# Kernel tuning notes

Hardware: AMD Instinct MI355X
Metric: run time of the kernel (lower is better)

## Reference

```python
import jax, jax.numpy as jnp
import numpy as np
from jax import lax

NUM_HEADS = 8
HEAD_DIM = 32
DIM = NUM_HEADS * HEAD_DIM  # 256
SR = 2
B, H, W = 4, 64, 64


def setup_inputs() -> dict:
    key = jax.random.key(0)
    ks = jax.random.split(key, 6)
    x = jax.random.normal(ks[0], (B, DIM, H, W), dtype=jnp.float32)
    # query: 1x1 conv without bias -> plain [out,in] matrix
    Wq = jax.random.normal(ks[1], (DIM, DIM), dtype=jnp.float32) * (1.0 / np.sqrt(DIM))
    # key/value: sr x sr conv, stride sr, no bias (OIHW)
    Wk = jax.random.normal(ks[2], (DIM, DIM, SR, SR), dtype=jnp.float32) * (1.0 / np.sqrt(DIM * SR * SR))
    Wv = jax.random.normal(ks[3], (DIM, DIM, SR, SR), dtype=jnp.float32) * (1.0 / np.sqrt(DIM * SR * SR))
    rel_h = jax.random.normal(ks[4], (1, NUM_HEADS, HEAD_DIM, 1, H // SR), dtype=jnp.float32)
    rel_w = jax.random.normal(ks[5], (1, NUM_HEADS, HEAD_DIM, W // SR, 1), dtype=jnp.float32)
    return {"x": x, "Wq": Wq, "Wk": Wk, "Wv": Wv, "rel_h": rel_h, "rel_w": rel_w}


def reference(x, Wq, Wk, Wv, rel_h, rel_w):
    b, c, h, w = x.shape
    nh, hd = NUM_HEADS, HEAD_DIM
    scale = hd ** (-0.5)
    dn = ('NCHW', 'OIHW', 'NCHW')

    # q: 1x1 conv == channel matmul; [B, C, H*W] -> [B, nh, hd, Nq]
    q = jnp.einsum('oc,bchw->bohw', Wq, x).reshape(b, nh, hd, h * w)
    # k, v: sr x sr conv, stride sr -> [B, nh, hd, Nkv]
    k = lax.conv_general_dilated(x, Wk, window_strides=(SR, SR), padding='VALID',
                                 dimension_numbers=dn).reshape(b, nh, hd, -1)
    v = lax.conv_general_dilated(x, Wv, window_strides=(SR, SR), padding='VALID',
                                 dimension_numbers=dn).reshape(b, nh, hd, -1)

    # attn scores: q^T k -> [B, nh, Nq, Nkv]
    attn = jnp.einsum('bhdn,bhdm->bhnm', q, k)
    # relative positional bias: (rel_h + rel_w) broadcast -> [nh, hd, Nkv]
    pos = (rel_h + rel_w).reshape(nh, hd, -1)
    attn = attn + jnp.einsum('bhdn,hdm->bhnm', q, pos)
    attn = jax.nn.softmax(attn * scale, axis=-1)

    # out = v @ attn^T -> [B, nh, hd, Nq] -> [B, C, H, W]
    out = jnp.einsum('bhdm,bhnm->bhdn', v, attn).reshape(b, c, h, w)
    return out
```

## Files before the change

kernel.cpp:

```cpp
#include <hip/hip_runtime.h>
#include <math.h>


typedef __bf16 bf16;
typedef __attribute__((ext_vector_type(4))) __bf16 bf16x4;
typedef __attribute__((ext_vector_type(8))) __bf16 bf16x8;
typedef __attribute__((ext_vector_type(4))) float f32x4;
typedef __attribute__((ext_vector_type(2))) __fp16 fp16x2_raw;
typedef __attribute__((ext_vector_type(4))) _Float16 f16x4;

#define MFMA16 __builtin_amdgcn_mfma_f32_16x16x32_bf16
#define MFMA16H __builtin_amdgcn_mfma_f32_16x16x16f16

#define QSCALE 0.25503486f
#define SOFTMAX_SHIFT 10.0f

__global__ void k_prep_w(const float* __restrict__ Wq, const float* __restrict__ Wk,
                         const float* __restrict__ Wv,
                         bf16* __restrict__ Wq_bf, bf16* __restrict__ Wkv_bf) {
    int tid = blockIdx.x * 256 + threadIdx.x;
    int c = tid >> 8, i = tid & 255;
    const float* Wsrc = (c < 256) ? Wk : Wv;
    int cs = c & 255;
    f32x4 w4 = ((const f32x4*)Wsrc)[cs * 256 + i];
#pragma unroll
    for (int tap = 0; tap < 4; tap++)
        Wkv_bf[c * 1024 + tap * 256 + i] = (bf16)w4[tap];
    if (tid < 16384) {
        f32x4 q4 = ((const f32x4*)Wq)[tid];
        bf16x4 o;
#pragma unroll
        for (int e = 0; e < 4; e++) o[e] = (bf16)(q4[e] * QSCALE);
        *(bf16x4*)(Wq_bf + tid * 4) = o;
    }
}

__global__ void k_xT(const float* __restrict__ x, bf16* __restrict__ xT) {
    int b = blockIdx.z, c0 = blockIdx.y * 64, n0 = blockIdx.x * 64;
    __shared__ float tile[64][65];
    int t = threadIdx.x;
    const float* xp = x + (size_t)(b * 256 + c0) * 4096 + n0;
#pragma unroll
    for (int k2 = 0; k2 < 16; k2++) {
        int flat = k2 * 256 + t;
        int row = flat >> 6, col = flat & 63;
        tile[row][col] = xp[(size_t)row * 4096 + col];
    }
    __syncthreads();
    bf16* op = xT + (size_t)(b * 4096 + n0) * 256 + c0;
#pragma unroll
    for (int k2 = 0; k2 < 16; k2++) {
        int flat = k2 * 256 + t;
        int row = flat >> 6, col = flat & 63;
        op[(size_t)row * 256 + col] = (bf16)tile[col][row];
    }
}

__launch_bounds__(256)
__global__ void k_gemm_kv(const bf16* __restrict__ xT, const bf16* __restrict__ Wkv_bf,
                          const float* __restrict__ rel_h, const float* __restrict__ rel_w,
                          bf16* __restrict__ kpos_t, _Float16* __restrict__ v_td) {
    int b = blockIdx.z;
    int bx = blockIdx.x;
    int m0 = bx * 32;
    int c0w = blockIdx.y * 64 + (threadIdx.x >> 6) * 16;
    int t = threadIdx.x, l = t & 63;
    int lr = l & 15, lg = l >> 4;
    __shared__ __align__(16) bf16 Ps[2][32 * 264];
    const bf16* xb = xT + (size_t)b * 4096 * 256;
    int srow = t >> 3;
    int scu0 = (t & 7) * 4;
    uint4 pre[4];
#define LOAD_CHUNK(tap)                                                        \
    {                                                                          \
        int dy = (tap) >> 1, dx = (tap) & 1;                                   \
        const bf16* src = xb + (size_t)((2 * bx + dy) * 64 + 2 * srow + dx) * 256; \
        _Pragma("unroll")                                                      \
        for (int j = 0; j < 4; j++)                                            \
            pre[j] = *(const uint4*)(src + (scu0 + j) * 8);                    \
    }
#define WRITE_CHUNK(buf)                                                       \
    {                                                                          \
        bf16* dst = Ps[buf] + srow * 264 + scu0 * 8;                           \
        _Pragma("unroll")                                                      \
        for (int j = 0; j < 4; j++) *(uint4*)(dst + j * 8) = pre[j];           \
    }
    LOAD_CHUNK(0)
    WRITE_CHUNK(0)
    const bf16* Gkb = Wkv_bf + (size_t)(c0w + lr) * 1024 + lg * 8;
    const bf16* Gvb = Gkb + 256 * 1024;
    f32x4 accK[2] = {}, accV[2] = {};
    for (int ch = 0; ch < 4; ch++) {
        if (ch < 3) LOAD_CHUNK(ch + 1)
        __syncthreads();
        const bf16* P = Ps[ch & 1];
#pragma unroll
        for (int kk = 0; kk < 8; kk++) {
            bf16x8 pa0 = *(const bf16x8*)(P + lr * 264 + kk * 32 + lg * 8);
            bf16x8 pa1 = *(const bf16x8*)(P + (16 + lr) * 264 + kk * 32 + lg * 8);
            bf16x8 gk = *(const bf16x8*)(Gkb + ch * 256 + kk * 32);
            bf16x8 gv = *(const bf16x8*)(Gvb + ch * 256 + kk * 32);
            accK[0] = MFMA16(pa0, gk, accK[0], 0, 0, 0);
            accK[1] = MFMA16(pa1, gk, accK[1], 0, 0, 0);
            accV[0] = MFMA16(gv, pa0, accV[0], 0, 0, 0);
            accV[1] = MFMA16(gv, pa1, accV[1], 0, 0, 0);
        }
        if (ch < 3) {
            __syncthreads();
            WRITE_CHUNK((ch + 1) & 1)
        }
    }
    {
        int cc = c0w + lr;
        float rw = rel_w[cc * 32 + bx];
#pragma unroll
        for (int i = 0; i < 2; i++)
#pragma unroll
            for (int r = 0; r < 4; r++) {
                int ml = i * 16 + lg * 4 + r;
                float val = accK[i][r] + rw + rel_h[cc * 32 + ml];
                kpos_t[((size_t)(b * 8 + (cc >> 5)) * 1024 + m0 + ml) * 32 + (cc & 31)] = (bf16)val;
            }
    }
#pragma unroll
    for (int j = 0; j < 2; j++) {
        int m = m0 + j * 16 + lr;
#pragma unroll
        for (int r = 0; r < 4; r++) {
            int cc = c0w + lg * 4 + r;
            v_td[((size_t)(b * 8 + (cc >> 5)) * 32 + (cc & 31)) * 1024 + m] = (_Float16)accV[j][r];
        }
    }
#undef LOAD_CHUNK
#undef WRITE_CHUNK
}

__launch_bounds__(256)
__global__ void k_attn(const bf16* __restrict__ xT, const bf16* __restrict__ Wq_bf,
                       const bf16* __restrict__ kpos_t, const _Float16* __restrict__ v_td,
                       float* __restrict__ out) {
    int b = blockIdx.z, h = blockIdx.y;
    int t = threadIdx.x;
    int w = t >> 6, l = t & 63;
    int n0 = blockIdx.x * 128 + w * 32;
    int lr = l & 15, lg = l >> 4;
    const size_t bh = (size_t)(b * 8 + h);
    __shared__ __align__(16) bf16 Ks[2][128 * 32];
    __shared__ __align__(16) _Float16 Vs[2][32][136];
    const bf16* Kb = kpos_t + bh * 1024 * 32;
    const _Float16* Vb = v_td + bh * 32 * 1024;
    bf16* Qs = (bf16*)Ks + w * 1280;
    {
        const bf16* Aw = Wq_bf + (size_t)(h * 32 + lr) * 256 + lg * 8;
        const bf16* Bx = xT + (size_t)(b * 4096 + n0 + lr) * 256 + lg * 8;
        f32x4 aq[2][2] = {};
#pragma unroll
        for (int kk = 0; kk < 8; kk++) {
            bf16x8 a0 = *(const bf16x8*)(Aw + kk * 32);
            bf16x8 a1 = *(const bf16x8*)(Aw + 16 * 256 + kk * 32);
            bf16x8 b0 = *(const bf16x8*)(Bx + kk * 32);
            bf16x8 b1 = *(const bf16x8*)(Bx + 16 * 256 + kk * 32);
            aq[0][0] = MFMA16(a0, b0, aq[0][0], 0, 0, 0);
            aq[0][1] = MFMA16(a0, b1, aq[0][1], 0, 0, 0);
            aq[1][0] = MFMA16(a1, b0, aq[1][0], 0, 0, 0);
            aq[1][1] = MFMA16(a1, b1, aq[1][1], 0, 0, 0);
        }
#pragma unroll
        for (int i = 0; i < 2; i++)
#pragma unroll
            for (int j = 0; j < 2; j++) {
                bf16x4 pk;
#pragma unroll
                for (int r = 0; r < 4; r++) pk[r] = (bf16)aq[i][j][r];
                *(bf16x4*)(Qs + (j * 16 + lr) * 40 + i * 16 + lg * 4) = pk;
            }
    }
    bf16x8 bq0, bq1;
    {
        bf16x4 a0 = *(const bf16x4*)(Qs + lr * 40 + lg * 8);
        bf16x4 a1 = *(const bf16x4*)(Qs + lr * 40 + lg * 8 + 4);
        bf16x4 b0 = *(const bf16x4*)(Qs + (16 + lr) * 40 + lg * 8);
        bf16x4 b1 = *(const bf16x4*)(Qs + (16 + lr) * 40 + lg * 8 + 4);
#pragma unroll
        for (int e = 0; e < 4; e++) {
            bq0[e] = a0[e]; bq0[4 + e] = a1[e];
            bq1[e] = b0[e]; bq1[4 + e] = b1[e];
        }
    }
    __syncthreads();
#define STAGE(ch, buf)                                                         \
    {                                                                          \
        const uint4* ksrc = (const uint4*)(Kb + (size_t)(ch) * 128 * 32);      \
        _Pragma("unroll")                                                      \
        for (int j = 0; j < 2; j++) {                                          \
            int u = t + j * 256;                        \
            int m = u >> 2;                                                    \
            int phys = ((m >> 1) + (u & 3)) & 3;                               \
            *(uint4*)(&Ks[buf][m * 32 + phys * 8]) = ksrc[u];                  \
        }                                                                      \
        _Pragma("unroll")                                                      \
        for (int j = 0; j < 2; j++) {                                          \
            int u = t + j * 256;                        \
            *(uint4*)(&Vs[buf][u >> 4][(u & 15) * 8]) =                        \
                *(const uint4*)(Vb + (size_t)(u >> 4) * 1024 + (ch) * 128 +    \
                                (u & 15) * 8);                                 \
        }                                                                      \
    }
    STAGE(0, 0)
    f32x4 accO[2][2] = {};
    f32x4 accS0 = {}, accS1 = {};
    const f16x4 onesv = {(_Float16)1.f, (_Float16)1.f, (_Float16)1.f, (_Float16)1.f};
    const f32x4 zs = {-SOFTMAX_SHIFT, -SOFTMAX_SHIFT, -SOFTMAX_SHIFT, -SOFTMAX_SHIFT};
    const int koff = (((lr >> 1) + lg) & 3) * 8;
    for (int ch = 0; ch < 8; ch++) {
        __syncthreads();
        if (ch < 7) STAGE(ch + 1, (ch + 1) & 1)
        const bf16* Kc = Ks[ch & 1];
#pragma unroll
        for (int tt = 0; tt < 8; tt++) {
            bf16x8 ak = *(const bf16x8*)(Kc + (tt * 16 + lr) * 32 + koff);
            f32x4 s0 = MFMA16(ak, bq0, zs, 0, 0, 0);
            f32x4 s1 = MFMA16(ak, bq1, zs, 0, 0, 0);
            f16x4 p0, p1;
            {
                fp16x2_raw c01 = __builtin_amdgcn_cvt_pkrtz(
                    __builtin_amdgcn_exp2f(s0[0]), __builtin_amdgcn_exp2f(s0[1]));
                fp16x2_raw c23 = __builtin_amdgcn_cvt_pkrtz(
                    __builtin_amdgcn_exp2f(s0[2]), __builtin_amdgcn_exp2f(s0[3]));
                p0[0] = c01[0]; p0[1] = c01[1]; p0[2] = c23[0]; p0[3] = c23[1];
                fp16x2_raw d01 = __builtin_amdgcn_cvt_pkrtz(
                    __builtin_amdgcn_exp2f(s1[0]), __builtin_amdgcn_exp2f(s1[1]));
                fp16x2_raw d23 = __builtin_amdgcn_cvt_pkrtz(
                    __builtin_amdgcn_exp2f(s1[2]), __builtin_amdgcn_exp2f(s1[3]));
                p1[0] = d01[0]; p1[1] = d01[1]; p1[2] = d23[0]; p1[3] = d23[1];
            }
            f16x4 v0 = *(const f16x4*)(&Vs[ch & 1][lr][tt * 16 + lg * 4]);
            f16x4 v1 = *(const f16x4*)(&Vs[ch & 1][16 + lr][tt * 16 + lg * 4]);
            accO[0][0] = MFMA16H(p0, v0, accO[0][0], 0, 0, 0);
            accO[0][1] = MFMA16H(p0, v1, accO[0][1], 0, 0, 0);
            accS0      = MFMA16H(p0, onesv, accS0, 0, 0, 0);
            accO[1][0] = MFMA16H(p1, v0, accO[1][0], 0, 0, 0);
            accO[1][1] = MFMA16H(p1, v1, accO[1][1], 0, 0, 0);
            accS1      = MFMA16H(p1, onesv, accS1, 0, 0, 0);
        }
    }
#undef STAGE
    float inv0[4], inv1[4];
#pragma unroll
    for (int r = 0; r < 4; r++) {
        inv0[r] = 1.0f / accS0[r];
        inv1[r] = 1.0f / accS1[r];
    }
#pragma unroll
    for (int dt = 0; dt < 2; dt++) {
        int c = h * 32 + dt * 16 + lr;
        float* op0 = out + (size_t)(b * 256 + c) * 4096 + n0 + lg * 4;
        float* op1 = op0 + 16;
        f32x4 o0, o1;
#pragma unroll
        for (int r = 0; r < 4; r++) {
            o0[r] = accO[0][dt][r] * inv0[r];
            o1[r] = accO[1][dt][r] * inv1[r];
        }
        *(f32x4*)op0 = o0;
        *(f32x4*)op1 = o1;
    }
}

extern "C" void kernel_launch(void* const* d_in, const int* in_sizes, int n_in,
                              void* d_out, int out_size, void* d_ws, size_t ws_size,
                              hipStream_t stream) {
    const float* x    = (const float*)d_in[0];
    const float* Wq   = (const float*)d_in[1];
    const float* Wk   = (const float*)d_in[2];
    const float* Wv   = (const float*)d_in[3];
    const float* relh = (const float*)d_in[4];
    const float* relw = (const float*)d_in[5];
    float* out = (float*)d_out;
    char* ws = (char*)d_ws;

    bf16*      xT     = (bf16*)(ws);
    bf16*      kposT  = (bf16*)(ws + (8u << 20));
    _Float16*  v_td   = (_Float16*)(ws + (10u << 20));
    bf16*      Wq_bf  = (bf16*)(ws + (12u << 20));
    bf16*      Wkv_bf = (bf16*)(ws + (12u << 20) + (256u << 10));

    k_prep_w <<<512,            256, 0, stream>>>(Wq, Wk, Wv, Wq_bf, Wkv_bf);
    k_xT     <<<dim3(64, 4, 4), 256, 0, stream>>>(x, xT);
    k_gemm_kv<<<dim3(32, 4, 4), 256, 0, stream>>>(xT, Wkv_bf, relh, relw, kposT, v_td);
    k_attn   <<<dim3(32, 8, 4), 256, 0, stream>>>(xT, Wq_bf, kposT, v_td, out);
}
```

Measured before the change: 155.6 us.

## Stage K/V tiles via direct global-to-LDS loads with swizzled V layout

Replaces register-staged global loads and LDS stores for the K and V chunks with global_load_lds async copies. Source addresses are permuted per lane so the LDS lands in a rotated/swizzled layout, dropping V's padded rows. The first V chunk is issued before the Q projection to overlap it. This removes VGPR round-trips and store instructions, but relies on correct swizzle index math and on the barrier waiting for the async LDS writes.

```diff
diff --git a/kernel.cpp b/kernel.cpp
--- a/kernel.cpp
+++ b/kernel.cpp
@@ -14,6 +14,12 @@
 
 #define QSCALE 0.25503486f
 #define SOFTMAX_SHIFT 10.0f
+
+typedef __attribute__((address_space(1))) const unsigned int gas_u32;
+typedef __attribute__((address_space(3))) unsigned int las_u32;
+__device__ __forceinline__ void gl_lds16(const void* g, void* s) {
+    __builtin_amdgcn_global_load_lds((gas_u32*)g, (las_u32*)s, 16, 0, 0);
+}
 
 __global__ void k_prep_w(const float* __restrict__ Wq, const float* __restrict__ Wk,
                          const float* __restrict__ Wv,
@@ -146,9 +152,32 @@
     int lr = l & 15, lg = l >> 4;
     const size_t bh = (size_t)(b * 8 + h);
     __shared__ __align__(16) bf16 Ks[2][128 * 32];
-    __shared__ __align__(16) _Float16 Vs[2][32][136];
+    __shared__ __align__(16) _Float16 Vs[2][32 * 128];
     const bf16* Kb = kpos_t + bh * 1024 * 32;
     const _Float16* Vb = v_td + bh * 32 * 1024;
+    const bf16* kg[2];
+    const _Float16* vg[2];
+#pragma unroll
+    for (int j = 0; j < 2; j++) {
+        int u = w * 128 + j * 64 + l;
+        int m = u >> 2, cg = ((u & 3) - (m >> 1)) & 3;
+        kg[j] = Kb + m * 32 + cg * 8;
+        int row = u >> 4, cl = ((u & 15) - row) & 15;
+        vg[j] = Vb + row * 1024 + cl * 8;
+    }
+#define STAGE_K(ch, buf)                                                       \
+    {                                                                          \
+        _Pragma("unroll")                                                      \
+        for (int j = 0; j < 2; j++)                                            \
+            gl_lds16(kg[j] + (ch) * 4096, &Ks[buf][(w * 128 + j * 64) * 8]);   \
+    }
+#define STAGE_V(ch, buf)                                                       \
+    {                                                                          \
+        _Pragma("unroll")                                                      \
+        for (int j = 0; j < 2; j++)                                            \
+            gl_lds16(vg[j] + (ch) * 128, &Vs[buf][(w * 128 + j * 64) * 8]);    \
+    }
+    STAGE_V(0, 0)
     bf16* Qs = (bf16*)Ks + w * 1280;
     {
         const bf16* Aw = Wq_bf + (size_t)(h * 32 + lr) * 256 + lg * 8;
@@ -188,34 +217,22 @@
         }
     }
     __syncthreads();
-#define STAGE(ch, buf)                                                         \
-    {                                                                          \
-        const uint4* ksrc = (const uint4*)(Kb + (size_t)(ch) * 128 * 32);      \
-        _Pragma("unroll")                                                      \
-        for (int j = 0; j < 2; j++) {                                          \
-            int u = t + j * 256;                        \
-            int m = u >> 2;                                                    \
-            int phys = ((m >> 1) + (u & 3)) & 3;                               \
-            *(uint4*)(&Ks[buf][m * 32 + phys * 8]) = ksrc[u];                  \
-        }                                                                      \
-        _Pragma("unroll")                                                      \
-        for (int j = 0; j < 2; j++) {                                          \
-            int u = t + j * 256;                        \
-            *(uint4*)(&Vs[buf][u >> 4][(u & 15) * 8]) =                        \
-                *(const uint4*)(Vb + (size_t)(u >> 4) * 1024 + (ch) * 128 +    \
-                                (u & 15) * 8);                                 \
-        }                                                                      \
-    }
-    STAGE(0, 0)
+    STAGE_K(0, 0)
     f32x4 accO[2][2] = {};
     f32x4 accS0 = {}, accS1 = {};
     const f16x4 onesv = {(_Float16)1.f, (_Float16)1.f, (_Float16)1.f, (_Float16)1.f};
     const f32x4 zs = {-SOFTMAX_SHIFT, -SOFTMAX_SHIFT, -SOFTMAX_SHIFT, -SOFTMAX_SHIFT};
     const int koff = (((lr >> 1) + lg) & 3) * 8;
+    const int vbase = lr * 128 + (lg & 1) * 4;
+    const int vrot = (lg >> 1) + lr;
     for (int ch = 0; ch < 8; ch++) {
         __syncthreads();
-        if (ch < 7) STAGE(ch + 1, (ch + 1) & 1)
+        if (ch < 7) {
+            STAGE_K(ch + 1, (ch + 1) & 1)
+            STAGE_V(ch + 1, (ch + 1) & 1)
+        }
         const bf16* Kc = Ks[ch & 1];
+        const _Float16* Vc = Vs[ch & 1];
 #pragma unroll
         for (int tt = 0; tt < 8; tt++) {
             bf16x8 ak = *(const bf16x8*)(Kc + (tt * 16 + lr) * 32 + koff);
@@ -234,8 +251,10 @@
                     __builtin_amdgcn_exp2f(s1[2]), __builtin_amdgcn_exp2f(s1[3]));
                 p1[0] = d01[0]; p1[1] = d01[1]; p1[2] = d23[0]; p1[3] = d23[1];
             }
-            f16x4 v0 = *(const f16x4*)(&Vs[ch & 1][lr][tt * 16 + lg * 4]);
-            f16x4 v1 = *(const f16x4*)(&Vs[ch & 1][16 + lr][tt * 16 + lg * 4]);
+            int cu = (2 * tt + vrot) & 15;
+            const _Float16* vp = Vc + vbase + cu * 8;
+            f16x4 v0 = *(const f16x4*)vp;
+            f16x4 v1 = *(const f16x4*)(vp + 2048);
             accO[0][0] = MFMA16H(p0, v0, accO[0][0], 0, 0, 0);
             accO[0][1] = MFMA16H(p0, v1, accO[0][1], 0, 0, 0);
             accS0      = MFMA16H(p0, onesv, accS0, 0, 0, 0);
@@ -244,7 +263,8 @@
             accS1      = MFMA16H(p1, onesv, accS1, 0, 0, 0);
         }
     }
-#undef STAGE
+#undef STAGE_K
+#undef STAGE_V
     float inv0[4], inv1[4];
 #pragma unroll
     for (int r = 0; r < 4; r++) {
```

New measurement: 155.9 us. About the same (+0.2%).
